# Performance work log

Hardware: AMD Instinct MI355X
Metric: run time of the kernel (lower is better)

The kernel has to match this reference:

```python
import jax, jax.numpy as jnp
import numpy as np

B, S1, S2 = 8, 2048, 2048
K1_DIM = K2_DIM = 512
PK1_DIM = PK2_DIM = 256
ATT_DIM = 512
DV = 512


def setup_inputs() -> dict:
    key = jax.random.key(0)
    ks = jax.random.split(key, 16)
    s = 0.02
    inp = {
        "k1": jax.random.normal(ks[0], (B, S1, K1_DIM), jnp.float32),
        "k2": jax.random.normal(ks[1], (B, S2, K2_DIM), jnp.float32),
        "preserved_k1": jax.random.normal(ks[2], (B, S1, PK1_DIM), jnp.float32),
        "preserved_k2": jax.random.normal(ks[3], (B, S2, PK2_DIM), jnp.float32),
        "v1": jax.random.normal(ks[4], (B, S1, DV), jnp.float32),
        "v2": jax.random.normal(ks[5], (B, S2, DV), jnp.float32),
        # Linear params stored as [in, out] (x @ W + b == torch Linear)
        "W_k1": jax.random.normal(ks[6], (K1_DIM, ATT_DIM), jnp.float32) * s,
        "b_k1": jnp.zeros((ATT_DIM,), jnp.float32),
        "W_k2": jax.random.normal(ks[7], (K2_DIM, ATT_DIM), jnp.float32) * s,
        "b_k2": jnp.zeros((ATT_DIM,), jnp.float32),
        "W_pk1": jax.random.normal(ks[8], (K1_DIM + PK1_DIM, ATT_DIM), jnp.float32) * s,
        "b_pk1": jnp.zeros((ATT_DIM,), jnp.float32),
        "W_pk2": jax.random.normal(ks[9], (K2_DIM + PK2_DIM, ATT_DIM), jnp.float32) * s,
        "b_pk2": jnp.zeros((ATT_DIM,), jnp.float32),
        # lengths in [S/2, S) so no softmax row is fully masked (original exits on NaN)
        "k1_lengths": jax.random.randint(ks[10], (B,), S1 // 2, S1, jnp.int32).astype(jnp.int64),
        "k2_lengths": jax.random.randint(ks[11], (B,), S2 // 2, S2, jnp.int32).astype(jnp.int64),
    }
    return inp


def _mask(k1_lengths, k2_lengths):
    # Faithful to the original loop: a position is masked iff EXACTLY ONE of
    # (row >= l1) / (col >= l2) holds (mask counter == 1, not >= 1).
    row_over = (jnp.arange(S1)[None, :, None] >= k1_lengths[:, None, None])  # [B,S1,1]
    col_over = (jnp.arange(S2)[None, None, :] >= k2_lengths[:, None, None])  # [B,1,S2]
    return (row_over.astype(jnp.int32) + col_over.astype(jnp.int32)) == 1  # [B,S1,S2]


def reference(k1, k2, preserved_k1, preserved_k2, v1, v2,
              W_k1, b_k1, W_k2, b_k2, W_pk1, b_pk1, W_pk2, b_pk2,
              k1_lengths, k2_lengths):
    pk1 = jnp.concatenate([k1, preserved_k1], axis=-1) @ W_pk1 + b_pk1  # [B,S1,A]
    pk2 = jnp.concatenate([k2, preserved_k2], axis=-1) @ W_pk2 + b_pk2  # [B,S2,A]
    k1p = k1 @ W_k1 + b_k1  # [B,S1,A]
    k2p = k2 @ W_k2 + b_k2  # [B,S2,A]

    score_1 = jnp.einsum("bsa,bta->bst", k1p, pk2)   # [B,S1,S2]
    score_2 = jnp.einsum("bsa,bta->bst", pk1, k2p)   # [B,S1,S2]

    mask = _mask(k1_lengths, k2_lengths)
    score_1 = jnp.where(mask, -jnp.inf, score_1)
    score_2 = jnp.where(mask, -jnp.inf, score_2)

    w1 = jax.nn.softmax(jnp.swapaxes(score_1, 1, 2), axis=-1)  # [B,S2,S1]
    w2 = jax.nn.softmax(score_2, axis=-1)                      # [B,S1,S2]

    o1 = jnp.einsum("bts,bsd->btd", w1, v1)  # [B,S2,DV]
    o2 = jnp.einsum("bst,btd->bsd", w2, v2)  # [B,S1,DV]
    # NOTE: original returns ragged per-sample slices of w1/w2; we return the
    # full padded weight matrices (slice w1[i,:l2,:l1], w2[i,:l1,:l2] to match).
    return (o1, o2, w1, w2)
```

## Files before the change

kernel.cpp:

```cpp
#include <hip/hip_runtime.h>

typedef _Float16 half8 __attribute__((ext_vector_type(8)));
typedef float    floatx4 __attribute__((ext_vector_type(4)));
typedef unsigned short u16;

constexpr int Bn  = 8;
constexpr int Sq  = 2048;
constexpr int KD  = 512;
constexpr int PKD = 256;
constexpr int AD  = 512;
constexpr int DV  = 512;

__global__ __launch_bounds__(256)
void transpose_cast_k(const float* __restrict__ in, _Float16* __restrict__ out,
                      int inRows, int inCols, long long bsIn, long long bsOut)
{
    __shared__ float t[32][33];
    const int b = blockIdx.z;
    in  += (long long)b * bsIn;
    out += (long long)b * bsOut;
    const int tx = threadIdx.x & 31;
    const int ty = threadIdx.x >> 5;
    const int c0 = blockIdx.x * 32;
    const int r0 = blockIdx.y * 32;
#pragma unroll
    for (int i = 0; i < 4; ++i)
        t[ty + 8*i][tx] = in[(long long)(r0 + ty + 8*i) * inCols + c0 + tx];
    __syncthreads();
#pragma unroll
    for (int i = 0; i < 4; ++i)
        out[(long long)(c0 + ty + 8*i) * inRows + r0 + tx] = (_Float16)t[tx][ty + 8*i];
}

template<bool A_F32, bool OUT_F16>
__global__ __launch_bounds__(256, 2)
void gemm_k(const void* __restrict__ A1v, const void* __restrict__ A2v, int Ksplit,
            int lda1, int lda2, long long bsA,
            const _Float16* __restrict__ Bm, int ldb, long long bsB,
            void* __restrict__ Cv, int ldc, long long bsC,
            const float* __restrict__ bias, int K)
{
    __shared__ __align__(16) _Float16 As[128][40];
    __shared__ __align__(16) _Float16 Bs[128][40];

    const int tid  = threadIdx.x;
    const int lane = tid & 63;
    const int wave = tid >> 6;
    const int wm   = (wave >> 1) * 64;
    const int wn   = (wave & 1) * 64;
    const int fr   = lane & 15;
    const int fq   = lane >> 4;

    const int tm = blockIdx.y, tn = blockIdx.x, bz = blockIdx.z;

    const int srow = tid >> 1;
    const int sseg = (tid & 1) * 16;

    const long long aRow = (long long)(tm * 128 + srow);
    const u16* Bsrc = (const u16*)(Bm + (long long)bz * bsB)
                    + (long long)(tn * 128 + srow) * ldb + sseg;

    floatx4 acc[4][4];
#pragma unroll
    for (int i = 0; i < 4; ++i)
#pragma unroll
        for (int j = 0; j < 4; ++j) acc[i][j] = (floatx4)0.0f;

    for (int k0 = 0; k0 < K; k0 += 32) {
        uint4 a0, a1;
        if (A_F32) {
            const int kk = k0 + sseg;
            const float* Ap;
            if (kk < Ksplit)
                Ap = (const float*)A1v + (long long)bz * bsA + aRow * lda1 + kk;
            else
                Ap = (const float*)A2v + aRow * lda2 + (kk - Ksplit);
            floatx4 f0 = *(const floatx4*)(Ap);
            floatx4 f1 = *(const floatx4*)(Ap + 4);
            floatx4 f2 = *(const floatx4*)(Ap + 8);
            floatx4 f3 = *(const floatx4*)(Ap + 12);
            union { _Float16 h[16]; uint4 q[2]; } av;
#pragma unroll
            for (int j = 0; j < 4; ++j) {
                av.h[j]      = (_Float16)f0[j];
                av.h[4 + j]  = (_Float16)f1[j];
                av.h[8 + j]  = (_Float16)f2[j];
                av.h[12 + j] = (_Float16)f3[j];
            }
            a0 = av.q[0]; a1 = av.q[1];
        } else {
            const u16* Ap = (const u16*)A1v + (long long)bz * bsA + aRow * lda1 + (k0 + sseg);
            a0 = *(const uint4*)Ap;
            a1 = *(const uint4*)(Ap + 8);
        }
        const u16* Bp = Bsrc + k0;
        const uint4 b0 = *(const uint4*)Bp;
        const uint4 b1 = *(const uint4*)(Bp + 8);

        __syncthreads();
        *(uint4*)&As[srow][sseg]     = a0;
        *(uint4*)&As[srow][sseg + 8] = a1;
        *(uint4*)&Bs[srow][sseg]     = b0;
        *(uint4*)&Bs[srow][sseg + 8] = b1;
        __syncthreads();

        half8 af[4], bf[4];
#pragma unroll
        for (int i = 0; i < 4; ++i) af[i] = *(const half8*)&As[wm + i*16 + fr][fq*8];
#pragma unroll
        for (int j = 0; j < 4; ++j) bf[j] = *(const half8*)&Bs[wn + j*16 + fr][fq*8];
#pragma unroll
        for (int i = 0; i < 4; ++i)
#pragma unroll
            for (int j = 0; j < 4; ++j)
                acc[i][j] = __builtin_amdgcn_mfma_f32_16x16x32_f16(af[i], bf[j], acc[i][j], 0, 0, 0);
    }

    const int crow0 = tm * 128 + wm + fq * 4;
    const int ccol0 = tn * 128 + wn + fr;
    if (OUT_F16) {
        _Float16* C = (_Float16*)Cv + (long long)bz * bsC;
#pragma unroll
        for (int i = 0; i < 4; ++i)
#pragma unroll
            for (int j = 0; j < 4; ++j) {
                const int col = ccol0 + j * 16;
                const float bv = bias[col];
#pragma unroll
                for (int r = 0; r < 4; ++r)
                    C[(long long)(crow0 + i*16 + r) * ldc + col] = (_Float16)(acc[i][j][r] + bv);
            }
    } else {
        float* C = (float*)Cv + (long long)bz * bsC;
#pragma unroll
        for (int i = 0; i < 4; ++i)
#pragma unroll
            for (int j = 0; j < 4; ++j) {
                const int col = ccol0 + j * 16;
#pragma unroll
                for (int r = 0; r < 4; ++r)
                    C[(long long)(crow0 + i*16 + r) * ldc + col] = acc[i][j][r];
            }
    }
}

__device__ __forceinline__ int load_len(const int* __restrict__ p, int b)
{
    return (p[1] == 0) ? p[2 * b] : p[b];
}

__global__ __launch_bounds__(256)
void softmax_mask_k(float* __restrict__ w, const int* __restrict__ lenR,
                    const int* __restrict__ lenC)
{
    const int b = blockIdx.y;
    const int r = blockIdx.x;
    float* row = w + ((long long)b * Sq + r) * (long long)Sq;
    const int lr = load_len(lenR, b);
    const int lc = load_len(lenC, b);
    const bool rover = (r >= lr);
    const int tid  = threadIdx.x;
    const int lane = tid & 63;
    const int wave = tid >> 6;

    floatx4 x0 = *(const floatx4*)(row + tid * 8);
    floatx4 x1 = *(const floatx4*)(row + tid * 8 + 4);
    float v[8];
#pragma unroll
    for (int j = 0; j < 4; ++j) { v[j] = x0[j]; v[4 + j] = x1[j]; }

    float m = -3.0e38f;
#pragma unroll
    for (int j = 0; j < 8; ++j) {
        const int c = tid * 8 + j;
        if (rover != (c >= lc)) v[j] = -__builtin_inff();
        m = fmaxf(m, v[j]);
    }
#pragma unroll
    for (int off = 32; off > 0; off >>= 1) m = fmaxf(m, __shfl_xor(m, off, 64));
    __shared__ float redm[4], reds[4];
    if (lane == 0) redm[wave] = m;
    __syncthreads();
    m = fmaxf(fmaxf(redm[0], redm[1]), fmaxf(redm[2], redm[3]));

    float s = 0.f;
#pragma unroll
    for (int j = 0; j < 8; ++j) { v[j] = __expf(v[j] - m); s += v[j]; }
#pragma unroll
    for (int off = 32; off > 0; off >>= 1) s += __shfl_xor(s, off, 64);
    if (lane == 0) reds[wave] = s;
    __syncthreads();
    s = reds[0] + reds[1] + reds[2] + reds[3];
    const float inv = 1.0f / s;
#pragma unroll
    for (int j = 0; j < 4; ++j) { x0[j] = v[j] * inv; x1[j] = v[4 + j] * inv; }
    *(floatx4*)(row + tid * 8)     = x0;
    *(floatx4*)(row + tid * 8 + 4) = x1;
}

extern "C" void kernel_launch(void* const* d_in, const int* in_sizes, int n_in,
                              void* d_out, int out_size, void* d_ws, size_t ws_size,
                              hipStream_t stream)
{
    (void)in_sizes; (void)n_in; (void)out_size; (void)ws_size;
    const float* k1    = (const float*)d_in[0];
    const float* k2    = (const float*)d_in[1];
    const float* pk1in = (const float*)d_in[2];
    const float* pk2in = (const float*)d_in[3];
    const float* v1    = (const float*)d_in[4];
    const float* v2    = (const float*)d_in[5];
    const float* W_k1  = (const float*)d_in[6];
    const float* b_k1  = (const float*)d_in[7];
    const float* W_k2  = (const float*)d_in[8];
    const float* b_k2  = (const float*)d_in[9];
    const float* W_pk1 = (const float*)d_in[10];
    const float* b_pk1 = (const float*)d_in[11];
    const float* W_pk2 = (const float*)d_in[12];
    const float* b_pk2 = (const float*)d_in[13];
    const int* len1 = (const int*)d_in[14];
    const int* len2 = (const int*)d_in[15];

    float* out = (float*)d_out;
    float* o1 = out;
    float* o2 = o1 + (long long)Bn * Sq * DV;
    float* w1 = o2 + (long long)Bn * Sq * DV;
    float* w2 = w1 + (long long)Bn * Sq * Sq;

    _Float16* k1p = (_Float16*)o1;
    _Float16* k2p = k1p + (long long)Bn * Sq * AD;
    _Float16* pk1 = (_Float16*)o2;
    _Float16* pk2 = pk1 + (long long)Bn * Sq * AD;

    _Float16* vT1   = (_Float16*)d_ws;
    _Float16* vT2   = vT1 + (long long)Bn * DV * Sq;
    _Float16* WTk1  = vT2 + (long long)Bn * DV * Sq;
    _Float16* WTk2  = WTk1 + AD * KD;
    _Float16* WTpk1 = WTk2 + AD * KD;
    _Float16* WTpk2 = WTpk1 + AD * (KD + PKD);

    transpose_cast_k<<<dim3(AD/32, KD/32, 1), 256, 0, stream>>>(W_k1, WTk1, KD, AD, 0, 0);
    transpose_cast_k<<<dim3(AD/32, KD/32, 1), 256, 0, stream>>>(W_k2, WTk2, KD, AD, 0, 0);
    transpose_cast_k<<<dim3(AD/32, (KD+PKD)/32, 1), 256, 0, stream>>>(W_pk1, WTpk1, KD+PKD, AD, 0, 0);
    transpose_cast_k<<<dim3(AD/32, (KD+PKD)/32, 1), 256, 0, stream>>>(W_pk2, WTpk2, KD+PKD, AD, 0, 0);
    transpose_cast_k<<<dim3(DV/32, Sq/32, Bn), 256, 0, stream>>>(v1, vT1, Sq, DV,
        (long long)Sq*DV, (long long)Sq*DV);
    transpose_cast_k<<<dim3(DV/32, Sq/32, Bn), 256, 0, stream>>>(v2, vT2, Sq, DV,
        (long long)Sq*DV, (long long)Sq*DV);

    const dim3 gProj(AD/128, (Bn*Sq)/128, 1);
    gemm_k<true, true><<<gProj, 256, 0, stream>>>(
        k1, nullptr, KD, KD, 0, 0,  WTk1, KD, 0,  k1p, AD, 0, b_k1, KD);
    gemm_k<true, true><<<gProj, 256, 0, stream>>>(
        k2, nullptr, KD, KD, 0, 0,  WTk2, KD, 0,  k2p, AD, 0, b_k2, KD);
    gemm_k<true, true><<<gProj, 256, 0, stream>>>(
        k1, pk1in, KD, KD, PKD, 0,  WTpk1, KD+PKD, 0,  pk1, AD, 0, b_pk1, KD+PKD);
    gemm_k<true, true><<<gProj, 256, 0, stream>>>(
        k2, pk2in, KD, KD, PKD, 0,  WTpk2, KD+PKD, 0,  pk2, AD, 0, b_pk2, KD+PKD);

    const dim3 gScore(Sq/128, Sq/128, Bn);
    gemm_k<false, false><<<gScore, 256, 0, stream>>>(
        pk2, nullptr, 0, AD, 0, (long long)Sq*AD,
        k1p, AD, (long long)Sq*AD,
        w1, Sq, (long long)Sq*Sq, nullptr, AD);
    gemm_k<false, false><<<gScore, 256, 0, stream>>>(
        pk1, nullptr, 0, AD, 0, (long long)Sq*AD,
        k2p, AD, (long long)Sq*AD,
        w2, Sq, (long long)Sq*Sq, nullptr, AD);

    softmax_mask_k<<<dim3(Sq, Bn), 256, 0, stream>>>(w1, len2, len1);
    softmax_mask_k<<<dim3(Sq, Bn), 256, 0, stream>>>(w2, len1, len2);

    const dim3 gOut(DV/128, Sq/128, Bn);
    gemm_k<true, false><<<gOut, 256, 0, stream>>>(
        w1, nullptr, Sq, Sq, 0, (long long)Sq*Sq,
        vT1, Sq, (long long)DV*Sq,
        o1, DV, (long long)Sq*DV, nullptr, Sq);
    gemm_k<true, false><<<gOut, 256, 0, stream>>>(
        w2, nullptr, Sq, Sq, 0, (long long)Sq*Sq,
        vT2, Sq, (long long)DV*Sq,
        o2, DV, (long long)Sq*DV, nullptr, Sq);
}
```

Baseline: 951.8 us.

## Stage GEMM tiles via direct global-to-LDS loads and emit fp16 softmax weights

The GEMM kernel now moves its A/B tiles with global_load_lds, writing straight into XOR-swizzled shared memory instead of going through registers. For fp32 A operands, the fp32 data is staged in LDS and converted to fp16 when fragments are read. The softmax kernel also writes a half-precision copy of the weights into workspace when the workspace is large enough, so the output GEMMs can read fp16 instead of fp32. This roughly halves their A-operand traffic, at the cost of an extra write pass and a dependence on the workspace size, with the old fp32 path kept as a fallback.

```diff
diff --git a/kernel.cpp b/kernel.cpp
--- a/kernel.cpp
+++ b/kernel.cpp
@@ -10,6 +10,13 @@
 constexpr int PKD = 256;
 constexpr int AD  = 512;
 constexpr int DV  = 512;
+
+__device__ __forceinline__ void llds16(const void* g, void* l)
+{
+    __builtin_amdgcn_global_load_lds(
+        (const __attribute__((address_space(1))) unsigned int*)g,
+        (__attribute__((address_space(3))) unsigned int*)l, 16, 0, 0);
+}
 
 __global__ __launch_bounds__(256)
 void transpose_cast_k(const float* __restrict__ in, _Float16* __restrict__ out,
@@ -40,8 +47,8 @@
             void* __restrict__ Cv, int ldc, long long bsC,
             const float* __restrict__ bias, int K)
 {
-    __shared__ __align__(16) _Float16 As[128][40];
-    __shared__ __align__(16) _Float16 Bs[128][40];
+    __shared__ __align__(16) unsigned char AsRaw[A_F32 ? 16384 : 8192];
+    __shared__ __align__(16) unsigned char BsRaw[8192];
 
     const int tid  = threadIdx.x;
     const int lane = tid & 63;
@@ -52,13 +59,9 @@
     const int fq   = lane >> 4;
 
     const int tm = blockIdx.y, tn = blockIdx.x, bz = blockIdx.z;
-
-    const int srow = tid >> 1;
-    const int sseg = (tid & 1) * 16;
-
-    const long long aRow = (long long)(tm * 128 + srow);
-    const u16* Bsrc = (const u16*)(Bm + (long long)bz * bsB)
-                    + (long long)(tn * 128 + srow) * ldb + sseg;
+    const long long aRowBase = (long long)tm * 128;
+    const long long bRowBase = (long long)tn * 128;
+    const _Float16* Bbase = Bm + (long long)bz * bsB;
 
     floatx4 acc[4][4];
 #pragma unroll
@@ -67,48 +70,77 @@
         for (int j = 0; j < 4; ++j) acc[i][j] = (floatx4)0.0f;
 
     for (int k0 = 0; k0 < K; k0 += 32) {
-        uint4 a0, a1;
+        __syncthreads();
+
         if (A_F32) {
-            const int kk = k0 + sseg;
-            const float* Ap;
-            if (kk < Ksplit)
-                Ap = (const float*)A1v + (long long)bz * bsA + aRow * lda1 + kk;
-            else
-                Ap = (const float*)A2v + aRow * lda2 + (kk - Ksplit);
-            floatx4 f0 = *(const floatx4*)(Ap);
-            floatx4 f1 = *(const floatx4*)(Ap + 4);
-            floatx4 f2 = *(const floatx4*)(Ap + 8);
-            floatx4 f3 = *(const floatx4*)(Ap + 12);
-            union { _Float16 h[16]; uint4 q[2]; } av;
+            const float* A1 = (const float*)A1v + (long long)bz * bsA;
+            const float* A2 = (const float*)A2v;
+#pragma unroll
+            for (int is = 0; is < 4; ++is) {
+                const int r  = (tid >> 3) + is * 32;
+                const int ch = (tid & 7) ^ (r & 7);
+                const int kk = k0 + ch * 4;
+                const float* src = (kk < Ksplit)
+                    ? A1 + (aRowBase + r) * lda1 + kk
+                    : A2 + (aRowBase + r) * lda2 + (kk - Ksplit);
+                llds16(src, AsRaw + tid * 16 + is * 4096);
+            }
+        } else {
+            const _Float16* A1 = (const _Float16*)A1v + (long long)bz * bsA;
+#pragma unroll
+            for (int is = 0; is < 2; ++is) {
+                const int r  = (tid >> 2) + is * 64;
+                const int ch = (tid & 3) ^ (r & 3);
+                llds16(A1 + (aRowBase + r) * lda1 + k0 + ch * 8,
+                       AsRaw + tid * 16 + is * 4096);
+            }
+        }
+#pragma unroll
+        for (int is = 0; is < 2; ++is) {
+            const int r  = (tid >> 2) + is * 64;
+            const int ch = (tid & 3) ^ (r & 3);
+            llds16(Bbase + (bRowBase + r) * ldb + k0 + ch * 8,
+                   BsRaw + tid * 16 + is * 4096);
+        }
+
+        __syncthreads();
+
+        half8 af[4], bf[4];
+        if (A_F32) {
+            const float* As32 = (const float*)AsRaw;
+#pragma unroll
+            for (int i = 0; i < 4; ++i) {
+                const int r  = wm + i * 16 + fr;
+                const int c0 = ((2 * fq) ^ (r & 7)) * 4;
+                const int c1 = ((2 * fq + 1) ^ (r & 7)) * 4;
+                floatx4 f0 = *(const floatx4*)(As32 + r * 32 + c0);
+                floatx4 f1 = *(const floatx4*)(As32 + r * 32 + c1);
+                half8 h;
+#pragma unroll
+                for (int j = 0; j < 4; ++j) {
+                    h[j]     = (_Float16)f0[j];
+                    h[4 + j] = (_Float16)f1[j];
+                }
+                af[i] = h;
+            }
+        } else {
+            const _Float16* As16 = (const _Float16*)AsRaw;
+#pragma unroll
+            for (int i = 0; i < 4; ++i) {
+                const int r  = wm + i * 16 + fr;
+                const int ch = fq ^ (r & 3);
+                af[i] = *(const half8*)(As16 + r * 32 + ch * 8);
+            }
+        }
+        {
+            const _Float16* Bs16 = (const _Float16*)BsRaw;
 #pragma unroll
             for (int j = 0; j < 4; ++j) {
-                av.h[j]      = (_Float16)f0[j];
-                av.h[4 + j]  = (_Float16)f1[j];
-                av.h[8 + j]  = (_Float16)f2[j];
-                av.h[12 + j] = (_Float16)f3[j];
-            }
-            a0 = av.q[0]; a1 = av.q[1];
-        } else {
-            const u16* Ap = (const u16*)A1v + (long long)bz * bsA + aRow * lda1 + (k0 + sseg);
-            a0 = *(const uint4*)Ap;
-            a1 = *(const uint4*)(Ap + 8);
+                const int r  = wn + j * 16 + fr;
+                const int ch = fq ^ (r & 3);
+                bf[j] = *(const half8*)(Bs16 + r * 32 + ch * 8);
+            }
         }
-        const u16* Bp = Bsrc + k0;
-        const uint4 b0 = *(const uint4*)Bp;
-        const uint4 b1 = *(const uint4*)(Bp + 8);
-
-        __syncthreads();
-        *(uint4*)&As[srow][sseg]     = a0;
-        *(uint4*)&As[srow][sseg + 8] = a1;
-        *(uint4*)&Bs[srow][sseg]     = b0;
-        *(uint4*)&Bs[srow][sseg + 8] = b1;
-        __syncthreads();
-
-        half8 af[4], bf[4];
-#pragma unroll
-        for (int i = 0; i < 4; ++i) af[i] = *(const half8*)&As[wm + i*16 + fr][fq*8];
-#pragma unroll
-        for (int j = 0; j < 4; ++j) bf[j] = *(const half8*)&Bs[wn + j*16 + fr][fq*8];
 #pragma unroll
         for (int i = 0; i < 4; ++i)
 #pragma unroll
@@ -150,12 +182,13 @@
 }
 
 __global__ __launch_bounds__(256)
-void softmax_mask_k(float* __restrict__ w, const int* __restrict__ lenR,
-                    const int* __restrict__ lenC)
+void softmax_mask_k(float* __restrict__ w, _Float16* __restrict__ wh,
+                    const int* __restrict__ lenR, const int* __restrict__ lenC)
 {
     const int b = blockIdx.y;
     const int r = blockIdx.x;
-    float* row = w + ((long long)b * Sq + r) * (long long)Sq;
+    const long long rowOff = ((long long)b * Sq + r) * (long long)Sq;
+    float* row = w + rowOff;
     const int lr = load_len(lenR, b);
     const int lc = load_len(lenC, b);
     const bool rover = (r >= lr);
@@ -196,13 +229,19 @@
     for (int j = 0; j < 4; ++j) { x0[j] = v[j] * inv; x1[j] = v[4 + j] * inv; }
     *(floatx4*)(row + tid * 8)     = x0;
     *(floatx4*)(row + tid * 8 + 4) = x1;
+    if (wh != nullptr) {
+        half8 h;
+#pragma unroll
+        for (int j = 0; j < 4; ++j) { h[j] = (_Float16)x0[j]; h[4 + j] = (_Float16)x1[j]; }
+        *(half8*)(wh + rowOff + tid * 8) = h;
+    }
 }
 
 extern "C" void kernel_launch(void* const* d_in, const int* in_sizes, int n_in,
                               void* d_out, int out_size, void* d_ws, size_t ws_size,
                               hipStream_t stream)
 {
-    (void)in_sizes; (void)n_in; (void)out_size; (void)ws_size;
+    (void)in_sizes; (void)n_in; (void)out_size;
     const float* k1    = (const float*)d_in[0];
     const float* k2    = (const float*)d_in[1];
     const float* pk1in = (const float*)d_in[2];
@@ -238,6 +277,13 @@
     _Float16* WTpk1 = WTk2 + AD * KD;
     _Float16* WTpk2 = WTpk1 + AD * (KD + PKD);
 
+    const unsigned long long fixedHalves =
+        2ull * Bn * DV * Sq + 2ull * AD * KD + 2ull * AD * (KD + PKD);
+    _Float16* w1h = (_Float16*)d_ws + fixedHalves;
+    _Float16* w2h = w1h + (long long)Bn * Sq * Sq;
+    const bool fast =
+        ws_size >= (fixedHalves + 2ull * Bn * Sq * Sq) * sizeof(_Float16);
+
     transpose_cast_k<<<dim3(AD/32, KD/32, 1), 256, 0, stream>>>(W_k1, WTk1, KD, AD, 0, 0);
     transpose_cast_k<<<dim3(AD/32, KD/32, 1), 256, 0, stream>>>(W_k2, WTk2, KD, AD, 0, 0);
     transpose_cast_k<<<dim3(AD/32, (KD+PKD)/32, 1), 256, 0, stream>>>(W_pk1, WTpk1, KD+PKD, AD, 0, 0);
@@ -249,9 +295,9 @@
 
     const dim3 gProj(AD/128, (Bn*Sq)/128, 1);
     gemm_k<true, true><<<gProj, 256, 0, stream>>>(
-        k1, nullptr, KD, KD, 0, 0,  WTk1, KD, 0,  k1p, AD, 0, b_k1, KD);
+        k1, k1, KD, KD, KD, 0,  WTk1, KD, 0,  k1p, AD, 0, b_k1, KD);
     gemm_k<true, true><<<gProj, 256, 0, stream>>>(
-        k2, nullptr, KD, KD, 0, 0,  WTk2, KD, 0,  k2p, AD, 0, b_k2, KD);
+        k2, k2, KD, KD, KD, 0,  WTk2, KD, 0,  k2p, AD, 0, b_k2, KD);
     gemm_k<true, true><<<gProj, 256, 0, stream>>>(
         k1, pk1in, KD, KD, PKD, 0,  WTpk1, KD+PKD, 0,  pk1, AD, 0, b_pk1, KD+PKD);
     gemm_k<true, true><<<gProj, 256, 0, stream>>>(
@@ -259,24 +305,35 @@
 
     const dim3 gScore(Sq/128, Sq/128, Bn);
     gemm_k<false, false><<<gScore, 256, 0, stream>>>(
-        pk2, nullptr, 0, AD, 0, (long long)Sq*AD,
+        pk2, pk2, 0, AD, AD, (long long)Sq*AD,
         k1p, AD, (long long)Sq*AD,
         w1, Sq, (long long)Sq*Sq, nullptr, AD);
     gemm_k<false, false><<<gScore, 256, 0, stream>>>(
-        pk1, nullptr, 0, AD, 0, (long long)Sq*AD,
+        pk1, pk1, 0, AD, AD, (long long)Sq*AD,
         k2p, AD, (long long)Sq*AD,
         w2, Sq, (long long)Sq*Sq, nullptr, AD);
 
-    softmax_mask_k<<<dim3(Sq, Bn), 256, 0, stream>>>(w1, len2, len1);
-    softmax_mask_k<<<dim3(Sq, Bn), 256, 0, stream>>>(w2, len1, len2);
+    softmax_mask_k<<<dim3(Sq, Bn), 256, 0, stream>>>(w1, fast ? w1h : nullptr, len2, len1);
+    softmax_mask_k<<<dim3(Sq, Bn), 256, 0, stream>>>(w2, fast ? w2h : nullptr, len1, len2);
 
     const dim3 gOut(DV/128, Sq/128, Bn);
-    gemm_k<true, false><<<gOut, 256, 0, stream>>>(
-        w1, nullptr, Sq, Sq, 0, (long long)Sq*Sq,
-        vT1, Sq, (long long)DV*Sq,
-        o1, DV, (long long)Sq*DV, nullptr, Sq);
-    gemm_k<true, false><<<gOut, 256, 0, stream>>>(
-        w2, nullptr, Sq, Sq, 0, (long long)Sq*Sq,
-        vT2, Sq, (long long)DV*Sq,
-        o2, DV, (long long)Sq*DV, nullptr, Sq);
-}
+    if (fast) {
+        gemm_k<false, false><<<gOut, 256, 0, stream>>>(
+            w1h, w1h, 0, Sq, Sq, (long long)Sq*Sq,
+            vT1, Sq, (long long)DV*Sq,
+            o1, DV, (long long)Sq*DV, nullptr, Sq);
+        gemm_k<false, false><<<gOut, 256, 0, stream>>>(
+            w2h, w2h, 0, Sq, Sq, (long long)Sq*Sq,
+            vT2, Sq, (long long)DV*Sq,
+            o2, DV, (long long)Sq*DV, nullptr, Sq);
+    } else {
+        gemm_k<true, false><<<gOut, 256, 0, stream>>>(
+            w1, w1, Sq, Sq, Sq, (long long)Sq*Sq,
+            vT1, Sq, (long long)DV*Sq,
+            o1, DV, (long long)Sq*DV, nullptr, Sq);
+        gemm_k<true, false><<<gOut, 256, 0, stream>>>(
+            w2, w2, Sq, Sq, Sq, (long long)Sq*Sq,
+            vT2, Sq, (long long)DV*Sq,
+            o2, DV, (long long)Sq*DV, nullptr, Sq);
+    }
+}
```

Result: no change. 935.0 us (-1.8%).
